# Performance work log

Hardware: AMD Instinct MI355X
Metric: run time of the kernel (lower is better)

Reference implementation:

```python
import jax, jax.numpy as jnp
import numpy as np

N = 20000      # nodes per graph
E = 640000     # edges per graph
FIN = 256      # input feature dim
H = 512        # hidden dim
K = 1000       # top_k


def _ln(x, g, b):
    m = jnp.mean(x, axis=-1, keepdims=True)
    v = jnp.var(x, axis=-1, keepdims=True)
    return (x - m) / jnp.sqrt(v + 1e-5) * g + b


def _gin_conv(x, src, dst, w1, b1, w2, b2):
    # GINConv with eps=0: mlp(x + sum_{j->i} x_j)
    agg = jax.ops.segment_sum(x[src], dst, num_segments=N)
    h = x + agg
    return jax.nn.relu(h @ w1 + b1) @ w2 + b2


def _gnn(x, edge_index, layers, lin_w, lin_b):
    src, dst = edge_index[0], edge_index[1]
    for (w1, b1, w2, b2) in layers:
        x = jax.nn.relu(_gin_conv(x, src, dst, w1, b1, w2, b2))
    return x @ lin_w + lin_b  # [N, 2]


def setup_inputs() -> dict:
    key = jax.random.key(0)
    ks = iter(jax.random.split(key, 40))
    w = lambda shape, s=0.02: jax.random.normal(next(ks), shape, jnp.float32) * s
    d = {}
    d["x1"] = jax.random.normal(next(ks), (N, FIN), jnp.float32)
    d["edge_index1"] = jax.random.randint(next(ks), (2, E), 0, N)
    d["x2"] = jax.random.normal(next(ks), (N, FIN), jnp.float32)
    d["edge_index2"] = jax.random.randint(next(ks), (2, E), 0, N)
    d["g_w11"] = w((FIN, H)); d["g_b11"] = jnp.zeros((H,), jnp.float32)
    d["g_w12"] = w((H, H));   d["g_b12"] = jnp.zeros((H,), jnp.float32)
    d["g_w21"] = w((H, H));   d["g_b21"] = jnp.zeros((H,), jnp.float32)
    d["g_w22"] = w((H, H));   d["g_b22"] = jnp.zeros((H,), jnp.float32)
    d["g_w31"] = w((H, H));   d["g_b31"] = jnp.zeros((H,), jnp.float32)
    d["g_w32"] = w((H, H));   d["g_b32"] = jnp.zeros((H,), jnp.float32)
    d["lin_w"] = w((H, 2));   d["lin_b"] = jnp.zeros((2,), jnp.float32)
    d["fc1_w"] = w((K, 128)); d["fc1_b"] = jnp.zeros((128,), jnp.float32)
    d["ln1_g"] = jnp.ones((128,), jnp.float32); d["ln1_b"] = jnp.zeros((128,), jnp.float32)
    d["fc2_w"] = w((128, H)); d["fc2_b"] = jnp.zeros((H,), jnp.float32)
    d["ln2_g"] = jnp.ones((H,), jnp.float32); d["ln2_b"] = jnp.zeros((H,), jnp.float32)
    d["fc3_w"] = w((H, 1));   d["fc3_b"] = jnp.zeros((1,), jnp.float32)
    return d


def reference(x1, edge_index1, x2, edge_index2,
              g_w11, g_b11, g_w12, g_b12,
              g_w21, g_b21, g_w22, g_b22,
              g_w31, g_b31, g_w32, g_b32,
              lin_w, lin_b,
              fc1_w, fc1_b, ln1_g, ln1_b,
              fc2_w, fc2_b, ln2_g, ln2_b,
              fc3_w, fc3_b):
    layers = [(g_w11, g_b11, g_w12, g_b12),
              (g_w21, g_b21, g_w22, g_b22),
              (g_w31, g_b31, g_w32, g_b32)]
    o1 = _gnn(x1, edge_index1, layers, lin_w, lin_b)  # [N, 2]
    o2 = _gnn(x2, edge_index2, layers, lin_w, lin_b)  # [N, 2]
    # torch.nn.PairwiseDistance(p=2, eps=1e-6): ||x1 - x2 + eps||_2 per row
    dist = jnp.sqrt(jnp.sum((o1 - o2 + 1e-6) ** 2, axis=-1))  # [N]
    vals, _ = jax.lax.top_k(dist, K)  # descending, matches torch.topk
    h = vals @ fc1_w + fc1_b
    h = jax.nn.relu(_ln(h, ln1_g, ln1_b))
    # dropout is identity in eval mode
    h = h @ fc2_w + fc2_b
    h = jax.nn.relu(_ln(h, ln2_g, ln2_b))
    return jax.nn.sigmoid(h @ fc3_w + fc3_b)  # [1]
```

## Files before the change

### kernel.cpp

```cpp
#include <hip/hip_runtime.h>
#include <hip/hip_bf16.h>
#include <math.h>

#define N1      20000
#define NT      40000
#define E1      640000
#define ET      1280000
#define FIN_D   256
#define HID_D   512
#define TOPK    1000
#define MP1     20096
#define NGEMM   628
#define AGG256  1250
#define AGG512  2500

#define NB       157
#define CAP      10240
#define BK_CHUNK 8192

typedef __attribute__((ext_vector_type(8))) short short8;
typedef __attribute__((ext_vector_type(4))) float floatx4;
typedef __attribute__((ext_vector_type(2))) float floatx2;
typedef unsigned int uintx4 __attribute__((ext_vector_type(4)));

__device__ __forceinline__ unsigned short f2bf(float f) {
    union { __hip_bfloat16 h; unsigned short u; } cv;
    cv.h = __float2bfloat16(f);
    return cv.u;
}
__device__ __forceinline__ float bflo(unsigned int u) {
    union { unsigned int i; float f; } c; c.i = u << 16; return c.f;
}
__device__ __forceinline__ float bfhi(unsigned int u) {
    union { unsigned int i; float f; } c; c.i = u & 0xffff0000u; return c.f;
}

__device__ __forceinline__ void convw_body(int bl, int K, float* tile ,
                                           const float* __restrict__ W,
                                           unsigned short* __restrict__ Wt) {
    int kb = K / 32;
    int k0 = (bl % kb) * 32, n0 = (bl / kb) * 32;
    int tx = threadIdx.x & 31, ty = threadIdx.x >> 5;
    for (int r = ty; r < 32; r += 8) tile[r * 33 + tx] = W[(size_t)(k0 + r) * HID_D + n0 + tx];
    __syncthreads();
    for (int r = ty; r < 32; r += 8)
        Wt[(size_t)(n0 + r) * K + k0 + tx] = f2bf(tile[tx * 33 + r]);
}
__device__ __forceinline__ void convx_body(int i, const float* __restrict__ x,
                                           unsigned short* __restrict__ xb,
                                           unsigned char* __restrict__ x8) {
    float4 f = ((const float4*)x)[i];
    ushort4 u;
    u.x = f2bf(f.x); u.y = f2bf(f.y); u.z = f2bf(f.z); u.w = f2bf(f.w);
    ((ushort4*)xb)[i] = u;
    int p = __builtin_amdgcn_cvt_pk_fp8_f32(f.x, f.y, 0, false);
    p = __builtin_amdgcn_cvt_pk_fp8_f32(f.z, f.w, p, true);
    ((unsigned int*)x8)[i] = (unsigned int)p;
}

__device__ __forceinline__ void bucketA_body(int bb, int t,
                                             const int* __restrict__ ei1,
                                             const int* __restrict__ ei2,
                                             unsigned int* __restrict__ stageG,
                                             int* __restrict__ gcnt,
                                             unsigned int* shb) {
    unsigned int* stg   = shb;
    unsigned int* scn   = shb + 8192;
    unsigned int* hoff  = shb + 8448;
    unsigned int* hcur  = shb + 8608;
    unsigned int* hbase = shb + 8768;
    int e0 = bb * BK_CHUNK;
    int total = ET - e0; if (total > BK_CHUNK) total = BK_CHUNK;
    for (int i = t; i < 160; i += 256) hcur[i] = 0;
    __syncthreads();
    for (int k = 0; k < 32; ++k) {
        int e = e0 + k * 256 + t;
        if (e < ET) {
            int d = (e < E1) ? ei1[E1 + e] : (ei2[E1 + (e - E1)] + N1);
            atomicAdd(&hcur[d >> 8], 1u);
        }
    }
    __syncthreads();
    unsigned int v = (t < NB) ? hcur[t] : 0u;
    scn[t] = v; __syncthreads();
    for (int off = 1; off < 256; off <<= 1) {
        unsigned int x = (t >= off) ? scn[t - off] : 0u;
        __syncthreads(); scn[t] += x; __syncthreads();
    }
    if (t < NB) {
        unsigned int ex = scn[t] - v;
        hoff[t] = ex;
        hbase[t] = (unsigned int)atomicAdd(&gcnt[t], (int)v);
    }
    __syncthreads();
    if (t < NB) hcur[t] = hoff[t];
    __syncthreads();
    for (int k = 0; k < 32; ++k) {
        int e = e0 + k * 256 + t;
        if (e < ET) {
            int s, d;
            if (e < E1) { s = ei1[e]; d = ei1[E1 + e]; }
            else        { int ee = e - E1; s = ei2[ee] + N1; d = ei2[E1 + ee] + N1; }
            unsigned int b8 = (unsigned int)(d >> 8);
            unsigned int pos = atomicAdd(&hcur[b8], 1u);
            stg[pos] = (unsigned int)s | ((unsigned int)(d & 255) << 16) | (b8 << 24);
        }
    }
    __syncthreads();
    for (int i = t; i < total; i += 256) {
        unsigned int e = stg[i];
        unsigned int b8 = e >> 24;
        unsigned int g = hbase[b8] + ((unsigned int)i - hoff[b8]);
        if (g < CAP) stageG[(size_t)b8 * CAP + g] = e;
    }
}

__launch_bounds__(256)
__global__ void prep_kernel(const int* __restrict__ ei1, const int* __restrict__ ei2,
                            unsigned int* __restrict__ stageG, int* __restrict__ gcnt,
                            const float* w11, unsigned short* wt11,
                            const float* w12, unsigned short* wt12,
                            const float* w21, unsigned short* wt21,
                            const float* w22, unsigned short* wt22,
                            const float* w31, unsigned short* wt31,
                            const float* w32, unsigned short* wt32,
                            const float* x1, const float* x2,
                            unsigned short* xb, unsigned char* x8) {
    __shared__ unsigned int shb[8928];
    int b = blockIdx.x;
    if (b < NB) { bucketA_body(b, threadIdx.x, ei1, ei2, stageG, gcnt, shb); }
    else if (b < NB + 128)  { convw_body(b - NB,          FIN_D, (float*)shb, w11, wt11); }
    else if (b < NB + 384)  { convw_body(b - (NB + 128),  HID_D, (float*)shb, w12, wt12); }
    else if (b < NB + 640)  { convw_body(b - (NB + 384),  HID_D, (float*)shb, w21, wt21); }
    else if (b < NB + 896)  { convw_body(b - (NB + 640),  HID_D, (float*)shb, w22, wt22); }
    else if (b < NB + 1152) { convw_body(b - (NB + 896),  HID_D, (float*)shb, w31, wt31); }
    else if (b < NB + 1408) { convw_body(b - (NB + 1152), HID_D, (float*)shb, w32, wt32); }
    else if (b < NB + 6408) { convx_body((b - (NB + 1408)) * 256 + threadIdx.x, x1, xb, x8); }
    else                    { convx_body((b - (NB + 6408)) * 256 + threadIdx.x, x2,
                                         xb + (size_t)N1 * FIN_D, x8 + (size_t)N1 * FIN_D); }
}

__launch_bounds__(256)
__global__ void sort_kernel(const unsigned int* __restrict__ stageG,
                            const int* __restrict__ gcnt,
                            int* __restrict__ row_start,
                            unsigned short* __restrict__ csr) {
    __shared__ unsigned int cnts[256], offs[256], cur[256], scn[256];
    __shared__ unsigned short outb[CAP];
    __shared__ int s_base;
    int b = blockIdx.x, t = threadIdx.x;
    unsigned int gv = (t < NB) ? (unsigned int)gcnt[t] : 0u;
    scn[t] = gv; __syncthreads();
    for (int off = 1; off < 256; off <<= 1) {
        unsigned int x = (t >= off) ? scn[t - off] : 0u;
        __syncthreads(); scn[t] += x; __syncthreads();
    }
    if (t == b) s_base = (int)(scn[t] - gv);
    cnts[t] = 0;
    __syncthreads();
    int base = s_base;
    int cnt = gcnt[b]; if (cnt > CAP) cnt = CAP;
    const unsigned int* src = stageG + (size_t)b * CAP;
    for (int i = t; i < cnt; i += 256) atomicAdd(&cnts[(src[i] >> 16) & 255], 1u);
    __syncthreads();
    unsigned int v = cnts[t];
    offs[t] = v; __syncthreads();
    for (int off = 1; off < 256; off <<= 1) {
        unsigned int x = (t >= off) ? offs[t - off] : 0u;
        __syncthreads(); offs[t] += x; __syncthreads();
    }
    unsigned int excl = offs[t] - v;
    cur[t] = excl;
    int node = b * 256 + t;
    if (node < NT) row_start[node] = base + (int)excl;
    if (b == 0 && t == 0) row_start[NT] = ET;
    __syncthreads();
    for (int i = t; i < cnt; i += 256) {
        unsigned int e = src[i];
        unsigned int p = atomicAdd(&cur[(e >> 16) & 255], 1u);
        outb[p] = (unsigned short)(e & 0xffffu);
    }
    __syncthreads();
    for (int i = t; i < cnt; i += 256) csr[base + i] = outb[i];
}

#define ACC4(u) do { \
    acc2[0] += __builtin_amdgcn_cvt_pk_f32_fp8((int)(u).x, false); \
    acc2[1] += __builtin_amdgcn_cvt_pk_f32_fp8((int)(u).x, true);  \
    acc2[2] += __builtin_amdgcn_cvt_pk_f32_fp8((int)(u).y, false); \
    acc2[3] += __builtin_amdgcn_cvt_pk_f32_fp8((int)(u).y, true);  \
    acc2[4] += __builtin_amdgcn_cvt_pk_f32_fp8((int)(u).z, false); \
    acc2[5] += __builtin_amdgcn_cvt_pk_f32_fp8((int)(u).z, true);  \
    acc2[6] += __builtin_amdgcn_cvt_pk_f32_fp8((int)(u).w, false); \
    acc2[7] += __builtin_amdgcn_cvt_pk_f32_fp8((int)(u).w, true);  } while (0)

template<int LPR4, int NSLAB>
__device__ __forceinline__ void agg8_body(int ab, int tid,
                                          const unsigned char* __restrict__ x8,
                                          const int* __restrict__ row_start,
                                          const unsigned short* __restrict__ csr,
                                          unsigned short* __restrict__ h, int n0) {
    int slab = ab & (NSLAB - 1);
    int grp  = ab / NSLAB;
    int node = grp * 32 + (tid >> 3);
    int lanec = tid & 7;
    int chunk = slab * 8 + lanec;
    const uint4* Xc = (const uint4*)x8 + chunk;
    floatx2 acc2[8] = {};
    uint4 v = Xc[(size_t)node * LPR4];
    ACC4(v);
    int nid = n0 + node;
    int s = row_start[nid], e = row_start[nid + 1];
    int p = s;
    for (; p + 8 <= e; p += 8) {
        int m0 = (int)csr[p + 0] - n0, m1 = (int)csr[p + 1] - n0;
        int m2 = (int)csr[p + 2] - n0, m3 = (int)csr[p + 3] - n0;
        int m4 = (int)csr[p + 4] - n0, m5 = (int)csr[p + 5] - n0;
        int m6 = (int)csr[p + 6] - n0, m7 = (int)csr[p + 7] - n0;
        uint4 u0 = Xc[(size_t)m0 * LPR4];
        uint4 u1 = Xc[(size_t)m1 * LPR4];
        uint4 u2 = Xc[(size_t)m2 * LPR4];
        uint4 u3 = Xc[(size_t)m3 * LPR4];
        uint4 u4 = Xc[(size_t)m4 * LPR4];
        uint4 u5 = Xc[(size_t)m5 * LPR4];
        uint4 u6 = Xc[(size_t)m6 * LPR4];
        uint4 u7 = Xc[(size_t)m7 * LPR4];
        ACC4(u0); ACC4(u1); ACC4(u2); ACC4(u3);
        ACC4(u4); ACC4(u5); ACC4(u6); ACC4(u7);
    }
    for (; p + 2 <= e; p += 2) {
        int ma = (int)csr[p + 0] - n0, mb = (int)csr[p + 1] - n0;
        uint4 u0 = Xc[(size_t)ma * LPR4];
        uint4 u1 = Xc[(size_t)mb * LPR4];
        ACC4(u0); ACC4(u1);
    }
    if (p < e) {
        int ma = (int)csr[p] - n0;
        uint4 u0 = Xc[(size_t)ma * LPR4];
        ACC4(u0);
    }
    unsigned int ow[8];
#pragma unroll
    for (int i = 0; i < 8; ++i)
        ow[i] = (unsigned)f2bf(acc2[i].x) | ((unsigned)f2bf(acc2[i].y) << 16);
    uintx4 o0, o1;
    o0.x = ow[0]; o0.y = ow[1]; o0.z = ow[2]; o0.w = ow[3];
    o1.x = ow[4]; o1.y = ow[5]; o1.z = ow[6]; o1.w = ow[7];
    size_t base = ((size_t)node * LPR4 + chunk) * 2;
    ((uintx4*)h)[base + 0] = o0;
    ((uintx4*)h)[base + 1] = o1;
}

template<int LPR4, int NSLAB>
__launch_bounds__(256, 4)
__global__ void agg_kernel(const unsigned char* __restrict__ x8,
                           const int* __restrict__ row_start,
                           const unsigned short* __restrict__ csr,
                           unsigned short* __restrict__ h, int n0) {
    agg8_body<LPR4, NSLAB>(blockIdx.x, threadIdx.x, x8, row_start, csr, h, n0);
}

__device__ __forceinline__ void store_fp8_tile(int row0, int col0, int tid,
                                               unsigned short* smem,
                                               floatx4 acc[4][4], const float* __restrict__ bias,
                                               unsigned char* __restrict__ C8,
                                               int wr, int wc, int lane) {
    unsigned char* tile = (unsigned char*)smem;
    int q = lane >> 4, cn = lane & 15;
#pragma unroll
    for (int j = 0; j < 4; ++j) {
        int lcol = wc * 64 + j * 16 + cn;
        float bv = bias[col0 + lcol];
#pragma unroll
        for (int i = 0; i < 4; ++i) {
            int lrow = wr * 64 + i * 16 + q * 4;
#pragma unroll
            for (int r = 0; r < 4; ++r) {
                float vv = fmaxf(acc[i][j][r] + bv, 0.f);
                int t8 = __builtin_amdgcn_cvt_pk_fp8_f32(vv, 0.f, 0, false);
                tile[(lrow + r) * 128 + lcol] = (unsigned char)(t8 & 0xff);
            }
        }
    }
    __syncthreads();
#pragma unroll
    for (int it = 0; it < 4; ++it) {
        int idx = it * 256 + tid;
        int lrow = idx >> 3, c16 = idx & 7;
        *(uint4*)(C8 + (size_t)(row0 + lrow) * HID_D + col0 + c16 * 16) =
            *(const uint4*)(tile + lrow * 128 + c16 * 16);
    }
}

__device__ __forceinline__ void gemm_body64(int bx, int by, int tid,
                                            unsigned short* smem,
                                            const unsigned short* __restrict__ A,
                                            const unsigned short* __restrict__ Wt,
                                            const float* __restrict__ bias,
                                            unsigned short* __restrict__ C,
                                            unsigned char* __restrict__ C8, int K) {
    const int N = HID_D;
    unsigned short* As = smem;
    unsigned short* Bs = smem + 8192;
    int lane = tid & 63;
    int w = tid >> 6;
    int wr = w >> 1, wc = w & 1;
    int row0 = bx * 128;
    int col0 = by * 128;
    floatx4 acc[4][4] = {};
    int lr = tid >> 3;
    int c8 = (tid & 7) * 8;
    const unsigned short* Ag = A + (size_t)row0 * K;
    const unsigned short* Bg = Wt + (size_t)col0 * K;

    for (int kt = 0; kt < K; kt += 64) {
#pragma unroll
        for (int l = 0; l < 4; ++l) {
            int r = l * 32 + lr;
            __builtin_amdgcn_global_load_lds(
                (const __attribute__((address_space(1))) void*)(Ag + (size_t)r * K + kt + c8),
                (__attribute__((address_space(3))) void*)(As + l * 2048 + tid * 8),
                16, 0, 0);
            __builtin_amdgcn_global_load_lds(
                (const __attribute__((address_space(1))) void*)(Bg + (size_t)r * K + kt + c8),
                (__attribute__((address_space(3))) void*)(Bs + l * 2048 + tid * 8),
                16, 0, 0);
        }
        __syncthreads();
#pragma unroll
        for (int kb = 0; kb < 2; ++kb) {
            short8 af[4], bf[4];
            int q8 = kb * 32 + (lane >> 4) * 8;
#pragma unroll
            for (int i = 0; i < 4; ++i) {
                int m = wr * 64 + i * 16 + (lane & 15);
                af[i] = *(const short8*)&As[m * 64 + q8];
                int n = wc * 64 + i * 16 + (lane & 15);
                bf[i] = *(const short8*)&Bs[n * 64 + q8];
            }
#pragma unroll
            for (int i = 0; i < 4; ++i)
#pragma unroll
                for (int j = 0; j < 4; ++j)
                    acc[i][j] = __builtin_amdgcn_mfma_f32_16x16x32_bf16(af[i], bf[j], acc[i][j], 0, 0, 0);
        }
        __syncthreads();
    }
    if (C8) {
        store_fp8_tile(row0, col0, tid, smem, acc, bias, C8, wr, wc, lane);
        return;
    }
    int q = lane >> 4;
    int cn = lane & 15;
#pragma unroll
    for (int j = 0; j < 4; ++j) {
        int col = col0 + wc * 64 + j * 16 + cn;
        float bv = bias[col];
#pragma unroll
        for (int i = 0; i < 4; ++i) {
            int rowb = row0 + wr * 64 + i * 16 + q * 4;
#pragma unroll
            for (int r = 0; r < 4; ++r) {
                float vv = fmaxf(acc[i][j][r] + bv, 0.f);
                C[(size_t)(rowb + r) * N + col] = f2bf(vv);
            }
        }
    }
}

__launch_bounds__(256)
__global__ void gemm_pair(const unsigned short* __restrict__ A1,
                          const unsigned short* __restrict__ W1,
                          const float* __restrict__ b1,
                          unsigned short* __restrict__ C1, unsigned char* C81, int K1,
                          const unsigned short* __restrict__ A2,
                          const unsigned short* __restrict__ W2,
                          const float* __restrict__ b2,
                          unsigned short* __restrict__ C2, unsigned char* C82, int K2) {
    __shared__ unsigned short smem[16384];
    int b = blockIdx.x;
    if (b < NGEMM) {
        gemm_body64(b % 157, b / 157, threadIdx.x, smem, A1, W1, b1, C1, C81, K1);
    } else {
        b -= NGEMM;
        gemm_body64(b % 157, b / 157, threadIdx.x, smem, A2, W2, b2, C2, C82, K2);
    }
}

template<int LPR4, int NSLAB>
__launch_bounds__(256)
__global__ void fused_k(const unsigned short* __restrict__ A,
                        const unsigned short* __restrict__ Wt,
                        const float* __restrict__ bias,
                        unsigned short* __restrict__ C, unsigned char* C8, int K,
                        const unsigned char* __restrict__ x8,
                        const int* __restrict__ row_start,
                        const unsigned short* __restrict__ csr,
                        unsigned short* __restrict__ h, int n0, int nGemm) {
    __shared__ unsigned short smem[16384];
    int b = blockIdx.x;
    if (b < nGemm) {
        gemm_body64(b % 157, b / 157, threadIdx.x, smem, A, Wt, bias, C, C8, K);
    } else {
        agg8_body<LPR4, NSLAB>(b - nGemm, threadIdx.x, x8, row_start, csr, h, n0);
    }
}

__device__ __forceinline__ void lin_body(int bb, int tid, const unsigned short* __restrict__ A,
                                         const float* __restrict__ w, const float* __restrict__ b,
                                         float* __restrict__ o, int M) {
    int wave = tid >> 6;
    int lane = tid & 63;
    int row = bb * 4 + wave;
    if (row >= M) return;
    const uint4* Ar = (const uint4*)(A + (size_t)row * 512);
    uint4 u = Ar[lane];
    float f[8];
    f[0] = bflo(u.x); f[1] = bfhi(u.x); f[2] = bflo(u.y); f[3] = bfhi(u.y);
    f[4] = bflo(u.z); f[5] = bfhi(u.z); f[6] = bflo(u.w); f[7] = bfhi(u.w);
    float s0 = 0.f, s1 = 0.f;
#pragma unroll
    for (int j = 0; j < 8; ++j) {
        int base = (lane * 8 + j) * 2;
        s0 = fmaf(f[j], w[base + 0], s0);
        s1 = fmaf(f[j], w[base + 1], s1);
    }
#pragma unroll
    for (int off = 32; off > 0; off >>= 1) {
        s0 += __shfl_down(s0, off, 64);
        s1 += __shfl_down(s1, off, 64);
    }
    if (lane == 0) { o[row * 2] = s0 + b[0]; o[row * 2 + 1] = s1 + b[1]; }
}

__launch_bounds__(256)
__global__ void fused_gemmlin(const unsigned short* __restrict__ A,
                              const unsigned short* __restrict__ Wt,
                              const float* __restrict__ bias,
                              unsigned short* __restrict__ C, int K,
                              const unsigned short* __restrict__ L,
                              const float* __restrict__ lw, const float* __restrict__ lb,
                              float* __restrict__ o) {
    __shared__ unsigned short smem[16384];
    int b = blockIdx.x;
    if (b < NGEMM) {
        gemm_body64(b % 157, b / 157, threadIdx.x, smem, A, Wt, bias, C, nullptr, K);
    } else {
        lin_body(b - NGEMM, threadIdx.x, L, lw, lb, o, N1);
    }
}

__global__ void lin_dist_kernel(const unsigned short* __restrict__ A,
                                const float* __restrict__ w, const float* __restrict__ b,
                                const float* __restrict__ o1,
                                float* __restrict__ o2out,
                                float* __restrict__ dist) {
    int tid = threadIdx.x;
    int wave = tid >> 6;
    int lane = tid & 63;
    int row = blockIdx.x * 4 + wave;
    if (row >= N1) return;
    const uint4* Ar = (const uint4*)(A + (size_t)row * 512);
    uint4 u = Ar[lane];
    float f[8];
    f[0] = bflo(u.x); f[1] = bfhi(u.x); f[2] = bflo(u.y); f[3] = bfhi(u.y);
    f[4] = bflo(u.z); f[5] = bfhi(u.z); f[6] = bflo(u.w); f[7] = bfhi(u.w);
    float s0 = 0.f, s1 = 0.f;
#pragma unroll
    for (int j = 0; j < 8; ++j) {
        int base = (lane * 8 + j) * 2;
        s0 = fmaf(f[j], w[base + 0], s0);
        s1 = fmaf(f[j], w[base + 1], s1);
    }
#pragma unroll
    for (int off = 32; off > 0; off >>= 1) {
        s0 += __shfl_down(s0, off, 64);
        s1 += __shfl_down(s1, off, 64);
    }
    if (lane == 0) {
        float vx = s0 + b[0], vy = s1 + b[1];
        o2out[row * 2] = vx; o2out[row * 2 + 1] = vy;
        float2 a = ((const float2*)o1)[row];
        float d0 = a.x - vx + 1e-6f, d1 = a.y - vy + 1e-6f;
        dist[row] = sqrtf(d0 * d0 + d1 * d1);
    }
}

#define HBLK 20
#define HPB  1000
__launch_bounds__(256)
__global__ void hist_lds_kernel(const float* __restrict__ dist, int* __restrict__ hist) {
    __shared__ int lh[4096];
    int t = threadIdx.x;
    for (int i = t; i < 4096; i += 256) lh[i] = 0;
    __syncthreads();
    int base = blockIdx.x * HPB;
    for (int i = t; i < HPB; i += 256) {
        int idx = base + i;
        if (idx < N1) atomicAdd(&lh[__float_as_uint(dist[idx]) >> 19], 1);
    }
    __syncthreads();
    for (int i = t; i < 4096; i += 256) {
        int v = lh[i];
        if (v) atomicAdd(&hist[i], v);
    }
}

__global__ void selk_kernel(const int* __restrict__ hist, int* __restrict__ selout) {
    __shared__ int tile[256];
    int t = threadIdx.x;
    int running = 0;
    for (int tb = 0; tb < 16; ++tb) {
        int idx = 4095 - (tb * 256 + t);
        int v = hist[idx];
        tile[t] = v;
        __syncthreads();
        for (int off = 1; off < 256; off <<= 1) {
            int x = (t >= off) ? tile[t - off] : 0;
            __syncthreads();
            tile[t] += x;
            __syncthreads();
        }
        int incl = running + tile[t];
        if (incl >= TOPK && incl - v < TOPK) selout[0] = idx;
        running += tile[255];
        __syncthreads();
        if (running >= TOPK) break;
    }
}

__global__ void compact_kernel(const float* __restrict__ dist, const int* __restrict__ selout,
                               int* __restrict__ nc, float* __restrict__ cd, int* __restrict__ ci) {
    int i = blockIdx.x * blockDim.x + threadIdx.x;
    if (i >= N1) return;
    float d = dist[i];
    int b = (int)(__float_as_uint(d) >> 19);
    if (b >= selout[0]) {
        int p = atomicAdd(nc, 1);
        cd[p] = d;
        ci[p] = i;
    }
}

#define CCH 2048
__global__ void rankc_kernel(const float* __restrict__ cd, const int* __restrict__ ci,
                             const int* __restrict__ nc_p, float* __restrict__ vals) {
    __shared__ float ds[CCH];
    __shared__ int   di_[CCH];
    int nc = *nc_p;
    if (blockIdx.x * 256 >= nc) return;
    int t = threadIdx.x;
    int q = blockIdx.x * 256 + t;
    float dq = 0.f; int iq = 0;
    if (q < nc) { dq = cd[q]; iq = ci[q]; }
    int cnt = 0;
    for (int c0 = 0; c0 < nc; c0 += CCH) {
        int lim = min(CCH, nc - c0);
        for (int j = t; j < lim; j += 256) { ds[j] = cd[c0 + j]; di_[j] = ci[c0 + j]; }
        __syncthreads();
        if (q < nc) {
            for (int j = 0; j < lim; ++j) {
                float dj = ds[j];
                cnt += (dj > dq) || (dj == dq && di_[j] < iq);
            }
        }
        __syncthreads();
    }
    if (q < nc && cnt < TOPK) vals[cnt] = dq;
}

__launch_bounds__(512)
__global__ void head_kernel(const float* __restrict__ vals,
                            const float* __restrict__ fc1_w, const float* __restrict__ fc1_b,
                            const float* __restrict__ ln1_g, const float* __restrict__ ln1_b,
                            const float* __restrict__ fc2_w, const float* __restrict__ fc2_b,
                            const float* __restrict__ ln2_g, const float* __restrict__ ln2_b,
                            const float* __restrict__ fc3_w, const float* __restrict__ fc3_b,
                            float* __restrict__ out) {
    __shared__ float sv[TOPK];
    __shared__ float a1[128];
    __shared__ float red[512];
    __shared__ float s_m, s_r;
    int t = threadIdx.x;
    for (int i = t; i < TOPK; i += 512) sv[i] = vals[i];
    __syncthreads();
    int g = t >> 7, c = t & 127;
    float part = 0.f;
    for (int j = g * 250; j < g * 250 + 250; ++j)
        part = fmaf(sv[j], fc1_w[j * 128 + c], part);
    red[t] = part;
    __syncthreads();
    float h1 = 0.f;
    if (t < 128) h1 = fc1_b[t] + red[t] + red[t + 128] + red[t + 256] + red[t + 384];
    __syncthreads();
    red[t] = (t < 128) ? h1 : 0.f; __syncthreads();
    for (int s = 256; s > 0; s >>= 1) { if (t < s) red[t] += red[t + s]; __syncthreads(); }
    if (t == 0) s_m = red[0] / 128.f;
    __syncthreads();
    float m1 = s_m;
    float dv = (t < 128) ? (h1 - m1) : 0.f;
    red[t] = dv * dv; __syncthreads();
    for (int s = 256; s > 0; s >>= 1) { if (t < s) red[t] += red[t + s]; __syncthreads(); }
    if (t == 0) s_r = rsqrtf(red[0] / 128.f + 1e-5f);
    __syncthreads();
    float r1 = s_r;
    if (t < 128) a1[t] = fmaxf((h1 - m1) * r1 * ln1_g[t] + ln1_b[t], 0.f);
    __syncthreads();
    float h2 = fc2_b[t];
    for (int j = 0; j < 128; ++j) h2 = fmaf(a1[j], fc2_w[j * 512 + t], h2);
    red[t] = h2; __syncthreads();
    for (int s = 256; s > 0; s >>= 1) { if (t < s) red[t] += red[t + s]; __syncthreads(); }
    if (t == 0) s_m = red[0] / 512.f;
    __syncthreads();
    float m2 = s_m;
    float d2 = h2 - m2;
    red[t] = d2 * d2; __syncthreads();
    for (int s = 256; s > 0; s >>= 1) { if (t < s) red[t] += red[t + s]; __syncthreads(); }
    if (t == 0) s_r = rsqrtf(red[0] / 512.f + 1e-5f);
    __syncthreads();
    float r2 = s_r;
    float y2 = fmaxf((h2 - m2) * r2 * ln2_g[t] + ln2_b[t], 0.f);
    red[t] = y2 * fc3_w[t]; __syncthreads();
    for (int s = 256; s > 0; s >>= 1) { if (t < s) red[t] += red[t + s]; __syncthreads(); }
    if (t == 0) out[0] = 1.f / (1.f + expf(-(red[0] + fc3_b[0])));
}

extern "C" void kernel_launch(void* const* d_in, const int* in_sizes, int n_in,
                              void* d_out, int out_size, void* d_ws, size_t ws_size,
                              hipStream_t stream) {
    const float* x1   = (const float*)d_in[0];
    const int*   ei1  = (const int*)d_in[1];
    const float* x2   = (const float*)d_in[2];
    const int*   ei2  = (const int*)d_in[3];
    const float* w11  = (const float*)d_in[4];
    const float* b11  = (const float*)d_in[5];
    const float* w12  = (const float*)d_in[6];
    const float* b12  = (const float*)d_in[7];
    const float* w21  = (const float*)d_in[8];
    const float* b21  = (const float*)d_in[9];
    const float* w22  = (const float*)d_in[10];
    const float* b22  = (const float*)d_in[11];
    const float* w31  = (const float*)d_in[12];
    const float* b31  = (const float*)d_in[13];
    const float* w32  = (const float*)d_in[14];
    const float* b32  = (const float*)d_in[15];
    const float* lw   = (const float*)d_in[16];
    const float* lb   = (const float*)d_in[17];
    const float* fc1w = (const float*)d_in[18];
    const float* fc1b = (const float*)d_in[19];
    const float* ln1g = (const float*)d_in[20];
    const float* ln1b = (const float*)d_in[21];
    const float* fc2w = (const float*)d_in[22];
    const float* fc2b = (const float*)d_in[23];
    const float* ln2g = (const float*)d_in[24];
    const float* ln2b = (const float*)d_in[25];
    const float* fc3w = (const float*)d_in[26];
    const float* fc3b = (const float*)d_in[27];

    char* ws = (char*)d_ws;
    size_t off = 0;
    auto alloc = [&](size_t bytes) -> void* {
        void* p = ws + off;
        off += (bytes + 255) & ~(size_t)255;
        return p;
    };
    unsigned short* XB  = (unsigned short*)alloc((size_t)NT * FIN_D * 2);
    unsigned char*  XB8 = (unsigned char*)alloc((size_t)NT * FIN_D);
    unsigned short* H0a = (unsigned short*)alloc((size_t)MP1 * HID_D * 2);
    unsigned short* H1a = (unsigned short*)alloc((size_t)MP1 * HID_D * 2);
    unsigned short* H0b = (unsigned short*)alloc((size_t)MP1 * HID_D * 2);
    unsigned short* H1b = (unsigned short*)alloc((size_t)MP1 * HID_D * 2);
    unsigned char*  F8a = (unsigned char*)alloc((size_t)MP1 * HID_D);
    unsigned char*  F8b = (unsigned char*)alloc((size_t)MP1 * HID_D);
    unsigned short* wt11 = (unsigned short*)alloc((size_t)HID_D * FIN_D * 2);
    unsigned short* wt12 = (unsigned short*)alloc((size_t)HID_D * HID_D * 2);
    unsigned short* wt21 = (unsigned short*)alloc((size_t)HID_D * HID_D * 2);
    unsigned short* wt22 = (unsigned short*)alloc((size_t)HID_D * HID_D * 2);
    unsigned short* wt31 = (unsigned short*)alloc((size_t)HID_D * HID_D * 2);
    unsigned short* wt32 = (unsigned short*)alloc((size_t)HID_D * HID_D * 2);
    float* o         = (float*)alloc((size_t)NT * 2 * 4);
    float* dist      = (float*)alloc((size_t)N1 * 4);
    float* vals      = (float*)alloc((size_t)TOPK * 4);
    int*   row_start = (int*)alloc((size_t)(NT + 1) * 4);
    unsigned short* csr16 = (unsigned short*)alloc((size_t)ET * 2);
    unsigned int* stageG  = (unsigned int*)alloc((size_t)NB * CAP * 4);
    int*   gcnt      = (int*)alloc((size_t)160 * 4);
    int*   selblk    = (int*)alloc((size_t)(4096 + 64) * 4);
    int*   hist      = selblk;
    int*   nc        = selblk + 4096;
    int*   selout    = (int*)alloc(2 * 4);
    float* cd        = (float*)alloc((size_t)N1 * 4);
    int*   ci        = (int*)alloc((size_t)N1 * 4);

    hipMemsetAsync(gcnt, 0, 160 * sizeof(int), stream);
    hipMemsetAsync(selblk, 0, (4096 + 64) * sizeof(int), stream);
    prep_kernel<<<NB + 1408 + 10000, 256, 0, stream>>>(ei1, ei2, stageG, gcnt,
                                                       w11, wt11, w12, wt12, w21, wt21,
                                                       w22, wt22, w31, wt31, w32, wt32,
                                                       x1, x2, XB, XB8);
    sort_kernel<<<NB, 256, 0, stream>>>(stageG, gcnt, row_start, csr16);

    const unsigned char* XB8g2 = XB8 + (size_t)N1 * FIN_D;

    agg_kernel<16, 2><<<AGG256, 256, 0, stream>>>(XB8, row_start, csr16, H0a, 0);
    fused_k<16, 2><<<NGEMM + AGG256, 256, 0, stream>>>(H0a, wt11, b11, H1a, nullptr, FIN_D,
                                                       XB8g2, row_start, csr16, H0b, N1, NGEMM);
    gemm_pair<<<2 * NGEMM, 256, 0, stream>>>(H1a, wt12, b12, nullptr, F8a, HID_D,
                                             H0b, wt11, b11, H1b, nullptr, FIN_D);
    fused_k<32, 4><<<NGEMM + AGG512, 256, 0, stream>>>(H1b, wt12, b12, nullptr, F8b, HID_D,
                                                       F8a, row_start, csr16, H1a, 0, NGEMM);
    fused_k<32, 4><<<NGEMM + AGG512, 256, 0, stream>>>(H1a, wt21, b21, H0a, nullptr, HID_D,
                                                       F8b, row_start, csr16, H1b, N1, NGEMM);
    gemm_pair<<<2 * NGEMM, 256, 0, stream>>>(H0a, wt22, b22, nullptr, F8a, HID_D,
                                             H1b, wt21, b21, H0b, nullptr, HID_D);
    fused_k<32, 4><<<NGEMM + AGG512, 256, 0, stream>>>(H0b, wt22, b22, nullptr, F8b, HID_D,
                                                       F8a, row_start, csr16, H1a, 0, NGEMM);
    fused_k<32, 4><<<NGEMM + AGG512, 256, 0, stream>>>(H1a, wt31, b31, H0a, nullptr, HID_D,
                                                       F8b, row_start, csr16, H1b, N1, NGEMM);
    gemm_pair<<<2 * NGEMM, 256, 0, stream>>>(H0a, wt32, b32, H1a, nullptr, HID_D,
                                             H1b, wt31, b31, H0b, nullptr, HID_D);
    fused_gemmlin<<<NGEMM + (N1 + 3) / 4, 256, 0, stream>>>(H0b, wt32, b32, H1b, HID_D,
                                                            H1a, lw, lb, o);
    lin_dist_kernel<<<(N1 + 3) / 4, 256, 0, stream>>>(H1b, lw, lb, o,
                                                      o + 2 * (size_t)N1, dist);
    hist_lds_kernel<<<HBLK, 256, 0, stream>>>(dist, hist);

    selk_kernel<<<1, 256, 0, stream>>>(hist, selout);
    compact_kernel<<<(N1 + 255) / 256, 256, 0, stream>>>(dist, selout, nc, cd, ci);
    rankc_kernel<<<(N1 + 255) / 256, 256, 0, stream>>>(cd, ci, nc, vals);
    head_kernel<<<1, 512, 0, stream>>>(vals, fc1w, fc1b, ln1g, ln1b,
                                       fc2w, fc2b, ln2g, ln2b, fc3w, fc3b,
                                       (float*)d_out);
}
```

Before: 752.8 us.

## Restage prep, sort and weight conversion; double-buffer GEMM K-loop

Removes the unused bf16 copy of the input features and splits preprocessing across kernels. The first graph's CSR sort now runs alongside conversion of x2, and the second graph's sort plus weight transposition run alongside the first aggregation, so independent work shares launches. The GEMM body changes from single-buffered 64-wide K tiles to double-buffered 32-wide tiles that prefetch the next tile during MFMA, with a bx/by block mapping. This relies on the layer-1 aggregation only reading graph-1 CSR rows sorted in the earlier kernel; halving the K tile also doubles the number of barriers.

```diff
diff --git a/kernel.cpp b/kernel.cpp
--- a/kernel.cpp
+++ b/kernel.cpp
@@ -15,6 +15,7 @@
 #define AGG512  2500
 
 #define NB       157
+#define NB_G1    79
 #define CAP      10240
 #define BK_CHUNK 8192
 
@@ -47,12 +48,8 @@
         Wt[(size_t)(n0 + r) * K + k0 + tx] = f2bf(tile[tx * 33 + r]);
 }
 __device__ __forceinline__ void convx_body(int i, const float* __restrict__ x,
-                                           unsigned short* __restrict__ xb,
                                            unsigned char* __restrict__ x8) {
     float4 f = ((const float4*)x)[i];
-    ushort4 u;
-    u.x = f2bf(f.x); u.y = f2bf(f.y); u.z = f2bf(f.z); u.w = f2bf(f.w);
-    ((ushort4*)xb)[i] = u;
     int p = __builtin_amdgcn_cvt_pk_fp8_f32(f.x, f.y, 0, false);
     p = __builtin_amdgcn_cvt_pk_fp8_f32(f.z, f.w, p, true);
     ((unsigned int*)x8)[i] = (unsigned int)p;
@@ -115,50 +112,28 @@
     }
 }
 
-__launch_bounds__(256)
-__global__ void prep_kernel(const int* __restrict__ ei1, const int* __restrict__ ei2,
-                            unsigned int* __restrict__ stageG, int* __restrict__ gcnt,
-                            const float* w11, unsigned short* wt11,
-                            const float* w12, unsigned short* wt12,
-                            const float* w21, unsigned short* wt21,
-                            const float* w22, unsigned short* wt22,
-                            const float* w31, unsigned short* wt31,
-                            const float* w32, unsigned short* wt32,
-                            const float* x1, const float* x2,
-                            unsigned short* xb, unsigned char* x8) {
-    __shared__ unsigned int shb[8928];
-    int b = blockIdx.x;
-    if (b < NB) { bucketA_body(b, threadIdx.x, ei1, ei2, stageG, gcnt, shb); }
-    else if (b < NB + 128)  { convw_body(b - NB,          FIN_D, (float*)shb, w11, wt11); }
-    else if (b < NB + 384)  { convw_body(b - (NB + 128),  HID_D, (float*)shb, w12, wt12); }
-    else if (b < NB + 640)  { convw_body(b - (NB + 384),  HID_D, (float*)shb, w21, wt21); }
-    else if (b < NB + 896)  { convw_body(b - (NB + 640),  HID_D, (float*)shb, w22, wt22); }
-    else if (b < NB + 1152) { convw_body(b - (NB + 896),  HID_D, (float*)shb, w31, wt31); }
-    else if (b < NB + 1408) { convw_body(b - (NB + 1152), HID_D, (float*)shb, w32, wt32); }
-    else if (b < NB + 6408) { convx_body((b - (NB + 1408)) * 256 + threadIdx.x, x1, xb, x8); }
-    else                    { convx_body((b - (NB + 6408)) * 256 + threadIdx.x, x2,
-                                         xb + (size_t)N1 * FIN_D, x8 + (size_t)N1 * FIN_D); }
-}
-
-__launch_bounds__(256)
-__global__ void sort_kernel(const unsigned int* __restrict__ stageG,
-                            const int* __restrict__ gcnt,
-                            int* __restrict__ row_start,
-                            unsigned short* __restrict__ csr) {
-    __shared__ unsigned int cnts[256], offs[256], cur[256], scn[256];
-    __shared__ unsigned short outb[CAP];
-    __shared__ int s_base;
-    int b = blockIdx.x, t = threadIdx.x;
+__device__ __forceinline__ void sort_body(int b, int t,
+                                          const unsigned int* __restrict__ stageG,
+                                          const int* __restrict__ gcnt,
+                                          int* __restrict__ row_start,
+                                          unsigned short* __restrict__ csr,
+                                          unsigned int* shb) {
+    unsigned int* cnts = shb;
+    unsigned int* offs = shb + 256;
+    unsigned int* cur  = shb + 512;
+    unsigned int* scn  = shb + 768;
+    unsigned short* outb = (unsigned short*)(shb + 1024);
+    int* s_base = (int*)(shb + 6144);
     unsigned int gv = (t < NB) ? (unsigned int)gcnt[t] : 0u;
     scn[t] = gv; __syncthreads();
     for (int off = 1; off < 256; off <<= 1) {
         unsigned int x = (t >= off) ? scn[t - off] : 0u;
         __syncthreads(); scn[t] += x; __syncthreads();
     }
-    if (t == b) s_base = (int)(scn[t] - gv);
+    if (t == b) s_base[0] = (int)(scn[t] - gv);
     cnts[t] = 0;
     __syncthreads();
-    int base = s_base;
+    int base = s_base[0];
     int cnt = gcnt[b]; if (cnt > CAP) cnt = CAP;
     const unsigned int* src = stageG + (size_t)b * CAP;
     for (int i = t; i < cnt; i += 256) atomicAdd(&cnts[(src[i] >> 16) & 255], 1u);
@@ -251,13 +226,58 @@
     ((uintx4*)h)[base + 1] = o1;
 }
 
-template<int LPR4, int NSLAB>
+__launch_bounds__(256)
+__global__ void prep1_kernel(const int* __restrict__ ei1, const int* __restrict__ ei2,
+                             unsigned int* __restrict__ stageG, int* __restrict__ gcnt,
+                             const float* __restrict__ x1, unsigned char* __restrict__ x8) {
+    __shared__ unsigned int shb[8928];
+    int b = blockIdx.x;
+    if (b < NB) bucketA_body(b, threadIdx.x, ei1, ei2, stageG, gcnt, shb);
+    else convx_body((b - NB) * 256 + threadIdx.x, x1, x8);
+}
+
+__launch_bounds__(256)
+__global__ void fused_sortx(const unsigned int* __restrict__ stageG,
+                            const int* __restrict__ gcnt,
+                            int* __restrict__ row_start,
+                            unsigned short* __restrict__ csr,
+                            const float* __restrict__ x2,
+                            unsigned char* __restrict__ x8g2) {
+    __shared__ unsigned int shb[6152];
+    int b = blockIdx.x;
+    if (b < NB_G1) sort_body(b, threadIdx.x, stageG, gcnt, row_start, csr, shb);
+    else convx_body((b - NB_G1) * 256 + threadIdx.x, x2, x8g2);
+}
+
 __launch_bounds__(256, 4)
-__global__ void agg_kernel(const unsigned char* __restrict__ x8,
-                           const int* __restrict__ row_start,
-                           const unsigned short* __restrict__ csr,
-                           unsigned short* __restrict__ h, int n0) {
-    agg8_body<LPR4, NSLAB>(blockIdx.x, threadIdx.x, x8, row_start, csr, h, n0);
+__global__ void fused_aggsw(const unsigned char* __restrict__ x8,
+                            int* __restrict__ row_start,
+                            unsigned short* __restrict__ csr,
+                            unsigned short* __restrict__ h,
+                            const unsigned int* __restrict__ stageG,
+                            const int* __restrict__ gcnt,
+                            const float* w11, unsigned short* wt11,
+                            const float* w12, unsigned short* wt12,
+                            const float* w21, unsigned short* wt21,
+                            const float* w22, unsigned short* wt22,
+                            const float* w31, unsigned short* wt31,
+                            const float* w32, unsigned short* wt32) {
+    __shared__ unsigned int shb[6152];
+    int b = blockIdx.x;
+    if (b < AGG256) {
+        agg8_body<16, 2>(b, threadIdx.x, x8, row_start, csr, h, 0);
+    } else if (b < AGG256 + (NB - NB_G1)) {
+        sort_body(b - AGG256 + NB_G1, threadIdx.x, stageG, gcnt, row_start, csr, shb);
+    } else {
+        int bl = b - (AGG256 + (NB - NB_G1));
+        float* tile = (float*)shb;
+        if (bl < 128)       convw_body(bl,        FIN_D, tile, w11, wt11);
+        else if (bl < 384)  convw_body(bl - 128,  HID_D, tile, w12, wt12);
+        else if (bl < 640)  convw_body(bl - 384,  HID_D, tile, w21, wt21);
+        else if (bl < 896)  convw_body(bl - 640,  HID_D, tile, w22, wt22);
+        else if (bl < 1152) convw_body(bl - 896,  HID_D, tile, w31, wt31);
+        else                convw_body(bl - 1152, HID_D, tile, w32, wt32);
+    }
 }
 
 __device__ __forceinline__ void store_fp8_tile(int row0, int col0, int tid,
@@ -292,58 +312,76 @@
     }
 }
 
-__device__ __forceinline__ void gemm_body64(int bx, int by, int tid,
-                                            unsigned short* smem,
-                                            const unsigned short* __restrict__ A,
-                                            const unsigned short* __restrict__ Wt,
-                                            const float* __restrict__ bias,
-                                            unsigned short* __restrict__ C,
-                                            unsigned char* __restrict__ C8, int K) {
+__device__ __forceinline__ void gemm_body_db(int bx, int by, int tid,
+                                             unsigned short* smem,
+                                             const unsigned short* __restrict__ A,
+                                             const unsigned short* __restrict__ Wt,
+                                             const float* __restrict__ bias,
+                                             unsigned short* __restrict__ C,
+                                             unsigned char* __restrict__ C8, int K) {
     const int N = HID_D;
-    unsigned short* As = smem;
-    unsigned short* Bs = smem + 8192;
     int lane = tid & 63;
     int w = tid >> 6;
     int wr = w >> 1, wc = w & 1;
     int row0 = bx * 128;
     int col0 = by * 128;
     floatx4 acc[4][4] = {};
-    int lr = tid >> 3;
-    int c8 = (tid & 7) * 8;
+    int lr = tid >> 2;
+    int c8 = (tid & 3) * 8;
     const unsigned short* Ag = A + (size_t)row0 * K;
     const unsigned short* Bg = Wt + (size_t)col0 * K;
-
-    for (int kt = 0; kt < K; kt += 64) {
-#pragma unroll
-        for (int l = 0; l < 4; ++l) {
-            int r = l * 32 + lr;
+    int nt = K >> 5;
+    {
+        unsigned short* As = smem;
+        unsigned short* Bs = smem + 4096;
+#pragma unroll
+        for (int l = 0; l < 2; ++l) {
+            int r = l * 64 + lr;
             __builtin_amdgcn_global_load_lds(
-                (const __attribute__((address_space(1))) void*)(Ag + (size_t)r * K + kt + c8),
+                (const __attribute__((address_space(1))) void*)(Ag + (size_t)r * K + c8),
                 (__attribute__((address_space(3))) void*)(As + l * 2048 + tid * 8),
                 16, 0, 0);
             __builtin_amdgcn_global_load_lds(
-                (const __attribute__((address_space(1))) void*)(Bg + (size_t)r * K + kt + c8),
+                (const __attribute__((address_space(1))) void*)(Bg + (size_t)r * K + c8),
                 (__attribute__((address_space(3))) void*)(Bs + l * 2048 + tid * 8),
                 16, 0, 0);
         }
-        __syncthreads();
-#pragma unroll
-        for (int kb = 0; kb < 2; ++kb) {
-            short8 af[4], bf[4];
-            int q8 = kb * 32 + (lane >> 4) * 8;
-#pragma unroll
-            for (int i = 0; i < 4; ++i) {
-                int m = wr * 64 + i * 16 + (lane & 15);
-                af[i] = *(const short8*)&As[m * 64 + q8];
-                int n = wc * 64 + i * 16 + (lane & 15);
-                bf[i] = *(const short8*)&Bs[n * 64 + q8];
+    }
+    __syncthreads();
+    for (int t = 0; t < nt; ++t) {
+        unsigned short* As = smem + ((t & 1) ? 8192 : 0);
+        unsigned short* Bs = As + 4096;
+        if (t + 1 < nt) {
+            unsigned short* An = smem + ((t & 1) ? 0 : 8192);
+            unsigned short* Bn = An + 4096;
+            int kt = (t + 1) << 5;
+#pragma unroll
+            for (int l = 0; l < 2; ++l) {
+                int r = l * 64 + lr;
+                __builtin_amdgcn_global_load_lds(
+                    (const __attribute__((address_space(1))) void*)(Ag + (size_t)r * K + kt + c8),
+                    (__attribute__((address_space(3))) void*)(An + l * 2048 + tid * 8),
+                    16, 0, 0);
+                __builtin_amdgcn_global_load_lds(
+                    (const __attribute__((address_space(1))) void*)(Bg + (size_t)r * K + kt + c8),
+                    (__attribute__((address_space(3))) void*)(Bn + l * 2048 + tid * 8),
+                    16, 0, 0);
             }
-#pragma unroll
-            for (int i = 0; i < 4; ++i)
-#pragma unroll
-                for (int j = 0; j < 4; ++j)
-                    acc[i][j] = __builtin_amdgcn_mfma_f32_16x16x32_bf16(af[i], bf[j], acc[i][j], 0, 0, 0);
-        }
+        }
+        short8 af[4], bf[4];
+        int q8 = (lane >> 4) * 8;
+#pragma unroll
+        for (int i = 0; i < 4; ++i) {
+            int m = wr * 64 + i * 16 + (lane & 15);
+            af[i] = *(const short8*)&As[m * 32 + q8];
+            int n = wc * 64 + i * 16 + (lane & 15);
+            bf[i] = *(const short8*)&Bs[n * 32 + q8];
+        }
+#pragma unroll
+        for (int i = 0; i < 4; ++i)
+#pragma unroll
+            for (int j = 0; j < 4; ++j)
+                acc[i][j] = __builtin_amdgcn_mfma_f32_16x16x32_bf16(af[i], bf[j], acc[i][j], 0, 0, 0);
         __syncthreads();
     }
     if (C8) {
@@ -380,10 +418,10 @@
     __shared__ unsigned short smem[16384];
     int b = blockIdx.x;
     if (b < NGEMM) {
-        gemm_body64(b % 157, b / 157, threadIdx.x, smem, A1, W1, b1, C1, C81, K1);
+        gemm_body_db(b >> 2, b & 3, threadIdx.x, smem, A1, W1, b1, C1, C81, K1);
     } else {
         b -= NGEMM;
-        gemm_body64(b % 157, b / 157, threadIdx.x, smem, A2, W2, b2, C2, C82, K2);
+        gemm_body_db(b >> 2, b & 3, threadIdx.x, smem, A2, W2, b2, C2, C82, K2);
     }
 }
 
@@ -400,7 +438,7 @@
     __shared__ unsigned short smem[16384];
     int b = blockIdx.x;
     if (b < nGemm) {
-        gemm_body64(b % 157, b / 157, threadIdx.x, smem, A, Wt, bias, C, C8, K);
+        gemm_body_db(b >> 2, b & 3, threadIdx.x, smem, A, Wt, bias, C, C8, K);
     } else {
         agg8_body<LPR4, NSLAB>(b - nGemm, threadIdx.x, x8, row_start, csr, h, n0);
     }
@@ -444,7 +482,7 @@
     __shared__ unsigned short smem[16384];
     int b = blockIdx.x;
     if (b < NGEMM) {
-        gemm_body64(b % 157, b / 157, threadIdx.x, smem, A, Wt, bias, C, nullptr, K);
+        gemm_body_db(b >> 2, b & 3, threadIdx.x, smem, A, Wt, bias, C, nullptr, K);
     } else {
         lin_body(b - NGEMM, threadIdx.x, L, lw, lb, o, N1);
     }
@@ -664,7 +702,6 @@
         off += (bytes + 255) & ~(size_t)255;
         return p;
     };
-    unsigned short* XB  = (unsigned short*)alloc((size_t)NT * FIN_D * 2);
     unsigned char*  XB8 = (unsigned char*)alloc((size_t)NT * FIN_D);
     unsigned short* H0a = (unsigned short*)alloc((size_t)MP1 * HID_D * 2);
     unsigned short* H1a = (unsigned short*)alloc((size_t)MP1 * HID_D * 2);
@@ -692,17 +729,17 @@
     float* cd        = (float*)alloc((size_t)N1 * 4);
     int*   ci        = (int*)alloc((size_t)N1 * 4);
 
+    const unsigned char* XB8g2 = XB8 + (size_t)N1 * FIN_D;
+
     hipMemsetAsync(gcnt, 0, 160 * sizeof(int), stream);
     hipMemsetAsync(selblk, 0, (4096 + 64) * sizeof(int), stream);
-    prep_kernel<<<NB + 1408 + 10000, 256, 0, stream>>>(ei1, ei2, stageG, gcnt,
-                                                       w11, wt11, w12, wt12, w21, wt21,
-                                                       w22, wt22, w31, wt31, w32, wt32,
-                                                       x1, x2, XB, XB8);
-    sort_kernel<<<NB, 256, 0, stream>>>(stageG, gcnt, row_start, csr16);
-
-    const unsigned char* XB8g2 = XB8 + (size_t)N1 * FIN_D;
-
-    agg_kernel<16, 2><<<AGG256, 256, 0, stream>>>(XB8, row_start, csr16, H0a, 0);
+    prep1_kernel<<<NB + 5000, 256, 0, stream>>>(ei1, ei2, stageG, gcnt, x1, XB8);
+    fused_sortx<<<NB_G1 + 5000, 256, 0, stream>>>(stageG, gcnt, row_start, csr16,
+                                                  x2, (unsigned char*)XB8g2);
+    fused_aggsw<<<AGG256 + (NB - NB_G1) + 1408, 256, 0, stream>>>(
+        XB8, row_start, csr16, H0a, stageG, gcnt,
+        w11, wt11, w12, wt12, w21, wt21, w22, wt22, w31, wt31, w32, wt32);
+
     fused_k<16, 2><<<NGEMM + AGG256, 256, 0, stream>>>(H0a, wt11, b11, H1a, nullptr, FIN_D,
                                                        XB8g2, row_start, csr16, H0b, N1, NGEMM);
     gemm_pair<<<2 * NGEMM, 256, 0, stream>>>(H1a, wt12, b12, nullptr, F8a, HID_D,
```

Result: no change. 739.0 us (-1.8%).
